# Kernel tuning notes

Measured on AMD Instinct MI355X. Metric: run time of the kernel, lower is better.

The kernel has to match this reference:

```python
import jax, jax.numpy as jnp
import numpy as np

N_NODES = 100000
N_EDGES = 1600000
D_FEAT = 64


def setup_inputs() -> dict:
    key = jax.random.key(0)
    k1, k2, k3 = jax.random.split(key, 3)
    features = jax.random.normal(k1, (N_NODES, D_FEAT), dtype=jnp.float32)
    row = jax.random.randint(k2, (N_EDGES,), 0, N_NODES, dtype=jnp.int64)
    col = jax.random.randint(k3, (N_EDGES,), 0, N_NODES, dtype=jnp.int64)
    return {"features": features, "row": row, "col": col, "index": 0}


def reference(features, row, col, index):
    # Symmetric normalization D^-1/2 A D^-1/2 with A having data == 1 (COO edges),
    # degrees taken from rowsums, exactly as normalize_adj() does.
    n = features.shape[0]
    deg = jax.ops.segment_sum(jnp.ones_like(row, dtype=features.dtype), row,
                              num_segments=n)  # [N]
    d_inv_sqrt = jnp.where(deg > 0, jax.lax.rsqrt(jnp.maximum(deg, 1e-30)), 0.0)
    vals = d_inv_sqrt[row] * d_inv_sqrt[col]  # [E] normalized edge weights
    # SpMM: out[r] = sum_{e: row[e]==r} vals[e] * features[col[e]]
    msgs = vals[:, None] * features[col]  # [E, D]
    out = jax.ops.segment_sum(msgs, row, num_segments=n)  # [N, D]
    return out
```

## Files before the change

### kernel.cpp

```cpp
#include <hip/hip_runtime.h>

#define DFEAT 64
#define RPB 128
#define RPB_SHIFT 7
#define KMAX 800
#define CAP 2816
#define BIN_CHUNK 4096
#define BIN_THREADS 512
#define EPT (BIN_CHUNK / BIN_THREADS)


__global__ __launch_bounds__(BIN_THREADS) void gcn_bin_kernel(
    const int* __restrict__ row, const int* __restrict__ col,
    unsigned* __restrict__ bucket_fill,
    int* __restrict__ pair_buf,
    int E, int K) {
    __shared__ unsigned cnt[KMAX];
    __shared__ unsigned resbase[KMAX];
    int tid = threadIdx.x;
    long long e0 = (long long)blockIdx.x * BIN_CHUNK;
    int nE = min(BIN_CHUNK, (int)(E - e0));

    for (int k = tid; k < K; k += BIN_THREADS) cnt[k] = 0u;
    __syncthreads();

    int      myr[EPT], myc[EPT];
    unsigned myrank[EPT];
    int ne = 0;
    for (int i = tid; i < nE; i += BIN_THREADS, ++ne) {
        int r = row[e0 + i];
        int c = col[e0 + i];
        myr[ne] = r;
        myc[ne] = c;
        myrank[ne] = atomicAdd(&cnt[r >> RPB_SHIFT], 1u);
    }
    __syncthreads();

    for (int k = tid; k < K; k += BIN_THREADS) {
        unsigned c = cnt[k];
        unsigned r = c ? atomicAdd(&bucket_fill[k], c) : 0u;
        resbase[k] = (unsigned)k * CAP + r;
    }
    __syncthreads();

    for (int j = 0; j < ne; ++j) {
        int k = myr[j] >> RPB_SHIFT;
        unsigned idx = resbase[k] + myrank[j];
        if (idx < (unsigned)(k + 1) * CAP)
            pair_buf[idx] = ((myr[j] & (RPB - 1)) << 17) | myc[j];
    }
}

__global__ __launch_bounds__(256) void gcn_rank_kernel(
    const int* __restrict__ pair_buf,
    const unsigned* __restrict__ bucket_fill,
    uint2* __restrict__ row_desc,
    float* __restrict__ dinv,
    int* __restrict__ col_sorted, int N, int K) {
    int k = blockIdx.x;
    int row0 = k << RPB_SHIFT;
    int rows_in = min(RPB, N - row0);
    __shared__ unsigned rcnt[RPB];
    __shared__ unsigned scan[RPB];
    __shared__ unsigned excl[RPB];
    __shared__ unsigned fillc[RPB];
    int tid = threadIdx.x;
    unsigned base = (unsigned)k * CAP;
    unsigned size = min(bucket_fill[k], (unsigned)CAP);

    if (tid < RPB) { rcnt[tid] = 0u; fillc[tid] = 0u; }
    __syncthreads();
    for (unsigned i = tid; i < size; i += 256)
        atomicAdd(&rcnt[pair_buf[base + i] >> 17], 1u);
    __syncthreads();
    if (tid < RPB) scan[tid] = rcnt[tid];
    __syncthreads();
    for (int off = 1; off < RPB; off <<= 1) {
        unsigned t = (tid < RPB && tid >= off) ? scan[tid - off] : 0u;
        __syncthreads();
        if (tid < RPB) scan[tid] += t;
        __syncthreads();
    }
    if (tid < RPB) excl[tid] = scan[tid] - rcnt[tid];
    __syncthreads();
    if (tid < rows_in) {
        unsigned s = base + excl[tid];
        unsigned d = rcnt[tid];
        row_desc[row0 + tid] = make_uint2(s, s + d);
        dinv[row0 + tid] = d ? rsqrtf((float)d) : 0.0f;
    }
    for (unsigned i = tid; i < size; i += 256) {
        int w = pair_buf[base + i];
        int lr = w >> 17;
        unsigned rank = atomicAdd(&fillc[lr], 1u);
        col_sorted[base + excl[lr] + rank] = w & 0x1FFFF;
    }
}

static __device__ inline unsigned short f2bf(float f) {
    unsigned u = __float_as_uint(f);
    unsigned r = (u + 0x7FFFu + ((u >> 16) & 1u)) >> 16;
    return (unsigned short)r;
}

__global__ __launch_bounds__(256) void gcn_tobf16_kernel(
    const float* __restrict__ feat, const float* __restrict__ dinv,
    unsigned short* __restrict__ wfeat, long long n4) {
    long long stride = (long long)gridDim.x * blockDim.x;
    for (long long i = blockIdx.x * (long long)blockDim.x + threadIdx.x;
         i < n4; i += stride) {
        int c = (int)(i >> 4);
        float w = dinv[c];
        float4 v = ((const float4*)feat)[i];
        ushort4 o;
        o.x = f2bf(w * v.x); o.y = f2bf(w * v.y);
        o.z = f2bf(w * v.z); o.w = f2bf(w * v.w);
        ((ushort4*)wfeat)[i] = o;
    }
}

static __device__ inline float bflo(unsigned u) {
    return __uint_as_float(u << 16);
}
static __device__ inline float bfhi(unsigned u) {
    return __uint_as_float(u & 0xFFFF0000u);
}

__global__ __launch_bounds__(256) void gcn_gather_bf16_kernel(
    const uint2* __restrict__ row_desc,
    const int* __restrict__ col_sorted,
    const unsigned short* __restrict__ wfeat,
    const float* __restrict__ dinv,
    float* __restrict__ out, int N) {
    int tid = threadIdx.x;
    int node = blockIdx.x * 16 + (tid >> 4);
    if (node >= N) return;
    int half = (tid >> 3) & 1;
    int sub = tid & 7;

    uint2 rd = row_desc[node];
    unsigned s = rd.x;
    unsigned e = rd.y;

    float a0 = 0.f, a1 = 0.f, a2 = 0.f, a3 = 0.f;
    float a4 = 0.f, a5 = 0.f, a6 = 0.f, a7 = 0.f;

#define FEAT16(C) (((const uint4*)(wfeat + (size_t)(C) * DFEAT))[sub])
#define ACC1(B) do { \
        a0 += bflo((B).x); a1 += bfhi((B).x); \
        a2 += bflo((B).y); a3 += bfhi((B).y); \
        a4 += bflo((B).z); a5 += bfhi((B).z); \
        a6 += bflo((B).w); a7 += bfhi((B).w); } while (0)

    unsigned j = s + half * 4u;
    int n0 = 0, n1 = 0, n2 = 0, n3 = 0;
    bool have = (j + 3 < e);
    if (have) {
        n0 = col_sorted[j];     n1 = col_sorted[j + 1];
        n2 = col_sorted[j + 2]; n3 = col_sorted[j + 3];
    }
    while (have) {
        int c0 = n0, c1 = n1, c2 = n2, c3 = n3;
        unsigned jn = j + 8;
        have = (jn + 3 < e);
        if (have) {
            n0 = col_sorted[jn];     n1 = col_sorted[jn + 1];
            n2 = col_sorted[jn + 2]; n3 = col_sorted[jn + 3];
        }
        uint4 b0 = FEAT16(c0);
        uint4 b1 = FEAT16(c1);
        uint4 b2 = FEAT16(c2);
        uint4 b3 = FEAT16(c3);
        ACC1(b0); ACC1(b1); ACC1(b2); ACC1(b3);
        j = jn;
    }
    for (; j < e; ++j) {
        uint4 b0 = FEAT16(col_sorted[j]);
        ACC1(b0);
    }
#undef FEAT16
#undef ACC1

    a0 += __shfl_xor(a0, 8, 64);
    a1 += __shfl_xor(a1, 8, 64);
    a2 += __shfl_xor(a2, 8, 64);
    a3 += __shfl_xor(a3, 8, 64);
    a4 += __shfl_xor(a4, 8, 64);
    a5 += __shfl_xor(a5, 8, 64);
    a6 += __shfl_xor(a6, 8, 64);
    a7 += __shfl_xor(a7, 8, 64);

    if (half == 0) {
        float wn = dinv[node];
        float4 o0 = make_float4(wn * a0, wn * a1, wn * a2, wn * a3);
        float4 o1 = make_float4(wn * a4, wn * a5, wn * a6, wn * a7);
        float4* op = (float4*)(out + (size_t)node * DFEAT + sub * 8);
        op[0] = o0;
        op[1] = o1;
    }
}


__global__ void gcn_deg_kernel(const int* __restrict__ row,
                               float* __restrict__ deg, int E) {
    int e = blockIdx.x * blockDim.x + threadIdx.x;
    if (e < E) atomicAdd(&deg[row[e]], 1.0f);
}

__global__ void gcn_rsqrt_kernel(float* __restrict__ deg, int N) {
    int i = blockIdx.x * blockDim.x + threadIdx.x;
    if (i < N) {
        float d = deg[i];
        deg[i] = (d > 0.0f) ? rsqrtf(d) : 0.0f;
    }
}

__global__ void gcn_scatter_kernel(const int* __restrict__ row,
                                   const int* __restrict__ col,
                                   const float* __restrict__ feat,
                                   const float* __restrict__ dinv,
                                   float* __restrict__ out, int E) {
    long long tid = (long long)blockIdx.x * blockDim.x + threadIdx.x;
    int e = (int)(tid >> 6);
    int d = (int)(tid & 63);
    if (e < E) {
        int r = row[e];
        int c = col[e];
        float v = dinv[r] * dinv[c];
        float x = feat[(long long)c * DFEAT + d];
        atomicAdd(&out[(long long)r * DFEAT + d], v * x);
    }
}

extern "C" void kernel_launch(void* const* d_in, const int* in_sizes, int n_in,
                              void* d_out, int out_size, void* d_ws, size_t ws_size,
                              hipStream_t stream) {
    const float* feat = (const float*)d_in[0];
    const int*   row  = (const int*)d_in[1];
    const int*   col  = (const int*)d_in[2];
    float* out = (float*)d_out;

    int N = in_sizes[0] / DFEAT;
    int E = in_sizes[1];
    int K = (N + RPB - 1) / RPB;

    size_t words = (size_t)KMAX + 2 * (size_t)N + (size_t)N + (size_t)K * CAP;
    size_t need = words * 4;
    size_t wf_off = (need + 15) & ~(size_t)15;
    size_t need_total = wf_off + (size_t)N * DFEAT * 2;
    bool pack_ok = (N <= (1 << 17)) && (K <= KMAX) &&
                   ((size_t)K * CAP <= (size_t)out_size);
    if (!pack_ok || ws_size < need_total) {
        float* deg = (float*)d_ws;
        (void)hipMemsetAsync(out, 0, (size_t)out_size * sizeof(float), stream);
        (void)hipMemsetAsync(deg, 0, (size_t)N * sizeof(float), stream);
        gcn_deg_kernel<<<(E + 255) / 256, 256, 0, stream>>>(row, deg, E);
        gcn_rsqrt_kernel<<<(N + 255) / 256, 256, 0, stream>>>(deg, N);
        long long total = (long long)E * DFEAT;
        gcn_scatter_kernel<<<(int)((total + 255) / 256), 256, 0, stream>>>(
            row, col, feat, deg, out, E);
        return;
    }

    unsigned* bucket_fill = (unsigned*)d_ws;
    uint2*    row_desc    = (uint2*)(bucket_fill + KMAX);
    float*    dinv        = (float*)(row_desc + N);
    int*      col_sorted  = (int*)(dinv + N);
    unsigned short* wfeat = (unsigned short*)((char*)d_ws + wf_off);
    int*      pair_buf    = (int*)d_out;

    (void)hipMemsetAsync(bucket_fill, 0, (size_t)KMAX * sizeof(unsigned),
                         stream);

    int binBlocks = (E + BIN_CHUNK - 1) / BIN_CHUNK;
    gcn_bin_kernel<<<binBlocks, BIN_THREADS, 0, stream>>>(row, col, bucket_fill,
                                                          pair_buf, E, K);
    gcn_rank_kernel<<<K, 256, 0, stream>>>(pair_buf, bucket_fill, row_desc,
                                           dinv, col_sorted, N, K);
    long long n4 = (long long)N * DFEAT / 4;
    gcn_tobf16_kernel<<<2048, 256, 0, stream>>>(feat, dinv, wfeat, n4);
    gcn_gather_bf16_kernel<<<(N + 15) / 16, 256, 0, stream>>>(
        row_desc, col_sorted, wfeat, dinv, out, N);
}
```

Baseline: 81.85 us.

## Fuse bf16 feature scaling into rank kernel and double rows per bucket

The separate kernel that scales features by the inverse square-root degree and converts them to bf16 is folded into the per-bucket rank kernel. Each bucket block now converts its own rows right after counting degrees, which removes a kernel launch and the extra read of dinv from global memory. Buckets also grow from 128 to 256 rows, with capacity doubled, so all 256 threads take part in the scan. Fewer, larger buckets mean about half as many rank blocks (~391 for 100k nodes), which may reduce parallelism across the GPU and make each block's serial work longer.

```diff
diff --git a/kernel.cpp b/kernel.cpp
--- a/kernel.cpp
+++ b/kernel.cpp
@@ -1,10 +1,10 @@
 #include <hip/hip_runtime.h>
 
 #define DFEAT 64
-#define RPB 128
-#define RPB_SHIFT 7
+#define RPB 256
+#define RPB_SHIFT 8
 #define KMAX 800
-#define CAP 2816
+#define CAP 5632
 #define BIN_CHUNK 4096
 #define BIN_THREADS 512
 #define EPT (BIN_CHUNK / BIN_THREADS)
@@ -51,12 +51,20 @@
     }
 }
 
+static __device__ inline unsigned short f2bf(float f) {
+    unsigned u = __float_as_uint(f);
+    unsigned r = (u + 0x7FFFu + ((u >> 16) & 1u)) >> 16;
+    return (unsigned short)r;
+}
+
 __global__ __launch_bounds__(256) void gcn_rank_kernel(
     const int* __restrict__ pair_buf,
     const unsigned* __restrict__ bucket_fill,
+    const float* __restrict__ feat,
     uint2* __restrict__ row_desc,
     float* __restrict__ dinv,
-    int* __restrict__ col_sorted, int N, int K) {
+    int* __restrict__ col_sorted,
+    unsigned short* __restrict__ wfeat, int N, int K) {
     int k = blockIdx.x;
     int row0 = k << RPB_SHIFT;
     int rows_in = min(RPB, N - row0);
@@ -68,20 +76,21 @@
     unsigned base = (unsigned)k * CAP;
     unsigned size = min(bucket_fill[k], (unsigned)CAP);
 
-    if (tid < RPB) { rcnt[tid] = 0u; fillc[tid] = 0u; }
+    rcnt[tid] = 0u;
+    fillc[tid] = 0u;
     __syncthreads();
     for (unsigned i = tid; i < size; i += 256)
         atomicAdd(&rcnt[pair_buf[base + i] >> 17], 1u);
     __syncthreads();
-    if (tid < RPB) scan[tid] = rcnt[tid];
+    scan[tid] = rcnt[tid];
     __syncthreads();
     for (int off = 1; off < RPB; off <<= 1) {
-        unsigned t = (tid < RPB && tid >= off) ? scan[tid - off] : 0u;
+        unsigned t = (tid >= off) ? scan[tid - off] : 0u;
         __syncthreads();
-        if (tid < RPB) scan[tid] += t;
+        scan[tid] += t;
         __syncthreads();
     }
-    if (tid < RPB) excl[tid] = scan[tid] - rcnt[tid];
+    excl[tid] = scan[tid] - rcnt[tid];
     __syncthreads();
     if (tid < rows_in) {
         unsigned s = base + excl[tid];
@@ -95,27 +104,17 @@
         unsigned rank = atomicAdd(&fillc[lr], 1u);
         col_sorted[base + excl[lr] + rank] = w & 0x1FFFF;
     }
-}
-
-static __device__ inline unsigned short f2bf(float f) {
-    unsigned u = __float_as_uint(f);
-    unsigned r = (u + 0x7FFFu + ((u >> 16) & 1u)) >> 16;
-    return (unsigned short)r;
-}
-
-__global__ __launch_bounds__(256) void gcn_tobf16_kernel(
-    const float* __restrict__ feat, const float* __restrict__ dinv,
-    unsigned short* __restrict__ wfeat, long long n4) {
-    long long stride = (long long)gridDim.x * blockDim.x;
-    for (long long i = blockIdx.x * (long long)blockDim.x + threadIdx.x;
-         i < n4; i += stride) {
-        int c = (int)(i >> 4);
-        float w = dinv[c];
-        float4 v = ((const float4*)feat)[i];
+    int total4 = rows_in * (DFEAT / 4);
+    for (int g = tid; g < total4; g += 256) {
+        int rl = g >> 4;
+        int j = g & 15;
+        unsigned d = rcnt[rl];
+        float w = d ? rsqrtf((float)d) : 0.0f;
+        float4 v = ((const float4*)(feat + (size_t)(row0 + rl) * DFEAT))[j];
         ushort4 o;
         o.x = f2bf(w * v.x); o.y = f2bf(w * v.y);
         o.z = f2bf(w * v.z); o.w = f2bf(w * v.w);
-        ((ushort4*)wfeat)[i] = o;
+        ((ushort4*)(wfeat + (size_t)(row0 + rl) * DFEAT))[j] = o;
     }
 }
 
@@ -275,10 +274,9 @@
     int binBlocks = (E + BIN_CHUNK - 1) / BIN_CHUNK;
     gcn_bin_kernel<<<binBlocks, BIN_THREADS, 0, stream>>>(row, col, bucket_fill,
                                                           pair_buf, E, K);
-    gcn_rank_kernel<<<K, 256, 0, stream>>>(pair_buf, bucket_fill, row_desc,
-                                           dinv, col_sorted, N, K);
-    long long n4 = (long long)N * DFEAT / 4;
-    gcn_tobf16_kernel<<<2048, 256, 0, stream>>>(feat, dinv, wfeat, n4);
+    gcn_rank_kernel<<<K, 256, 0, stream>>>(pair_buf, bucket_fill, feat,
+                                           row_desc, dinv, col_sorted,
+                                           wfeat, N, K);
     gcn_gather_bf16_kernel<<<(N + 15) / 16, 256, 0, stream>>>(
         row_desc, col_sorted, wfeat, dinv, out, N);
 }
```

Result: slower. 83.62 us (+2.2%).
